# Optimization experiments

Hardware: AMD Instinct MI355X
Metric: run time of the kernel (lower is better)

Reference implementation:

```python
import jax, jax.numpy as jnp
import numpy as np

B, S, D, H, E = 8, 2048, 1024, 4096, 8


def setup_inputs() -> dict:
    key = jax.random.key(0)
    k0, k1, k2, k3 = jax.random.split(key, 4)
    x = jax.random.normal(k0, (B, S, D), dtype=jnp.float32)
    # hash-router assignment: one expert per token, shape [B, S, 1] (top-k dim k=1)
    assign = jax.random.randint(k1, (B, S, 1), 0, E, dtype=jnp.int64)
    # per-expert Linear(dim, hidden): W_e [E, D, H], b_e [E, H]
    W_e = jax.random.normal(k2, (E, D, H), dtype=jnp.float32) * (1.0 / np.sqrt(D))
    b_e = jnp.zeros((E, H), dtype=jnp.float32)
    # shared output Linear(hidden, dim)
    W_out = jax.random.normal(k3, (H, D), dtype=jnp.float32) * (1.0 / np.sqrt(H))
    b_out = jnp.zeros((D,), dtype=jnp.float32)
    return {"x": x, "W_e": W_e, "b_e": b_e, "W_out": W_out, "b_out": b_out,
            "assign": assign}


def reference(x, W_e, b_e, W_out, b_out, assign):
    num_experts = W_e.shape[0]
    hidden = W_e.shape[2]
    # zero-init combine buffer, matching torch.zeros(batch, seq, hidden)
    expert_out = jnp.zeros(x.shape[:2] + (hidden,), dtype=x.dtype)
    for e in range(num_experts):  # fixed small expert loop
        y = jnp.einsum("bsd,dh->bsh", x, W_e[e]) + b_e[e]
        mask = (assign == e).any(-1)  # [B, S]
        expert_out = jnp.where(mask[..., None], y, expert_out)
    h = jax.nn.relu(expert_out)
    return jnp.einsum("bsh,hd->bsd", h, W_out) + b_out
```

## Files before the change

### kernel.cpp

```cpp
#include <hip/hip_runtime.h>
#include <hip/hip_bf16.h>
#include <stdint.h>

#define NB 8
#define NS 2048
#define ND 1024
#define NH 4096
#define NE 8
#define NTOK (NB*NS)

typedef __bf16 bf16;
typedef bf16 bf16x8 __attribute__((ext_vector_type(8)));
typedef float f32x4 __attribute__((ext_vector_type(4)));

static const size_t OFF_XB  = 128 * 1024;
static const size_t OFF_WTE = OFF_XB  + (size_t)NTOK * ND * 2;
static const size_t OFF_WTO = OFF_WTE + (size_t)NE * NH * ND * 2;
static const size_t OFF_HB  = OFF_WTO + (size_t)ND * NH * 2;
static const size_t WS_NEED = OFF_HB  + (size_t)NTOK * NH * 2;

#define GLDS16(src, dst) __builtin_amdgcn_global_load_lds( \
    (__attribute__((address_space(1))) void*)(void*)(src), \
    (__attribute__((address_space(3))) void*)(dst), 16, 0, 0)


__global__ void k_route(const int* __restrict__ assign, int* __restrict__ meta) {
    __shared__ int cnt[NE];
    __shared__ int offs_s[NE];
    int tid = threadIdx.x;
    if (tid < NE) cnt[tid] = 0;
    __syncthreads();
    for (int t = tid; t < NTOK; t += 1024) atomicAdd(&cnt[assign[t] & 7], 1);
    __syncthreads();
    if (tid == 0) {
        int o = 0;
        for (int e = 0; e < NE; e++) {
            meta[e] = cnt[e]; meta[16 + e] = o; offs_s[e] = o; o += cnt[e];
        }
    }
    __syncthreads();
    if (tid < NE) cnt[tid] = offs_s[tid];
    __syncthreads();
    int* perm = meta + 512;
    for (int t = tid; t < NTOK; t += 1024) {
        int e = assign[t] & 7;
        int p = atomicAdd(&cnt[e], 1);
        perm[p] = t;
    }
}

__global__ void k_gather_cvt(const float* __restrict__ x, const int* __restrict__ meta,
                             bf16* __restrict__ xbp) {
    long i = (long)blockIdx.x * blockDim.x + threadIdx.x;
    int row = (int)(i >> 7);
    int c8  = (int)(i & 127);
    const int* perm = meta + 512;
    int tok = perm[row];
    const float4* s = (const float4*)(x + (size_t)tok * ND + c8 * 8);
    float4 v0 = s[0], v1 = s[1];
    bf16x8 o;
    o[0] = (bf16)v0.x; o[1] = (bf16)v0.y; o[2] = (bf16)v0.z; o[3] = (bf16)v0.w;
    o[4] = (bf16)v1.x; o[5] = (bf16)v1.y; o[6] = (bf16)v1.z; o[7] = (bf16)v1.w;
    *(bf16x8*)(xbp + i * 8) = o;
}

__global__ void k_transpose(const float* __restrict__ in, bf16* __restrict__ out,
                            int R, int C) {
    __shared__ float tile[32][33];
    int b  = blockIdx.z;
    int c0 = blockIdx.x * 32, r0 = blockIdx.y * 32;
    const float* inb = in + (size_t)b * R * C;
    bf16* outb = out + (size_t)b * R * C;
    int tx = threadIdx.x, ty = threadIdx.y;
#pragma unroll
    for (int i = 0; i < 4; i++) {
        int r = r0 + ty + i * 8;
        tile[ty + i * 8][tx] = inb[(size_t)r * C + c0 + tx];
    }
    __syncthreads();
#pragma unroll
    for (int i = 0; i < 4; i++) {
        int c = c0 + ty + i * 8;
        outb[(size_t)c * R + r0 + tx] = (bf16)tile[tx][ty + i * 8];
    }
}


#define BAR { __builtin_amdgcn_s_barrier(); asm volatile("" ::: "memory"); }
#define VMC8 asm volatile("s_waitcnt vmcnt(8)" ::: "memory")
#define VMC0 asm volatile("s_waitcnt vmcnt(0)" ::: "memory")

#define LDA(msub) { \
  const char* Ab = sm + abuf + wr * 16384; \
  _Pragma("unroll") for (int m = 0; m < 4; m++) { \
    int row = ((msub) * 4 + m) * 16 + lr; \
    af[m][0] = *(const bf16x8*)(Ab + row * 128 + xk0); \
    af[m][1] = *(const bf16x8*)(Ab + row * 128 + xk1); \
  } }

#define LDB(nsub) { \
  const char* Bb = sm + bbuf + (wc >> 1) * 16384; \
  _Pragma("unroll") for (int n = 0; n < 2; n++) { \
    int row = (wc & 1) * 64 + ((nsub) * 2 + n) * 16 + lr; \
    bfr[(nsub)*2+n][0] = *(const bf16x8*)(Bb + row * 128 + xk0); \
    bfr[(nsub)*2+n][1] = *(const bf16x8*)(Bb + row * 128 + xk1); \
  } }

#define MFMA_Q(msub, nsub) { \
  __builtin_amdgcn_s_setprio(1); \
  _Pragma("unroll") for (int m = 0; m < 4; m++) \
  _Pragma("unroll") for (int n = 0; n < 2; n++) \
  _Pragma("unroll") for (int k = 0; k < 2; k++) \
    acc[(msub)*4+m][(nsub)*2+n] = __builtin_amdgcn_mfma_f32_16x16x32_bf16( \
        af[m][k], bfr[(nsub)*2+n][k], acc[(msub)*4+m][(nsub)*2+n], 0, 0, 0); \
  __builtin_amdgcn_s_setprio(0); }

#define DO_TILE(i, S0, S1, S2, S3, VW) { \
  const int abuf = ((i) % 3) * 32768; \
  const int bbuf = 98304 + ((i) & 1) * 32768; \
  LDA(0); LDB(0); S0; BAR; MFMA_Q(0,0); BAR; \
  LDB(1);         S1; BAR; MFMA_Q(0,1); BAR; \
  LDA(1);         S2; BAR; MFMA_Q(1,0); BAR; \
                  S3; VW; BAR; MFMA_Q(1,1); BAR; \
}

#define STAGE_A(t, h) { \
    char* d = sm + ((t) % 3) * 32768 + (h) * 16384 + wid * 1024; \
    GLDS16(srcA(t, h, 0), d); \
    GLDS16(srcA(t, h, 1), d + 8192); }
#define STAGE_B(t, h) { \
    char* d = sm + 98304 + ((t) & 1) * 32768 + (h) * 16384 + wid * 1024; \
    GLDS16(srcB(t, h, 0), d); \
    GLDS16(srcB(t, h, 1), d + 8192); }

__launch_bounds__(512, 2)
__global__ void k_gemm1(const bf16* __restrict__ xbp, const bf16* __restrict__ wte,
                        const float* __restrict__ b_e, bf16* __restrict__ hb,
                        const int* __restrict__ meta) {
    __shared__ __align__(16) char sm[163840];
    int f = blockIdx.x;
    int e = f & 7, q = f >> 3;
    int j = q % 9, bx = q / 9;
    int cnt = meta[e];
    int rs  = meta[16 + e] + j * 256;
    int rc  = cnt - j * 256; if (rc > 256) rc = 256;
    if (rc <= 0) return;
    int n0 = bx * 256;

    int tid = threadIdx.x;
    int lane = tid & 63, wid = tid >> 6;
    int wr = wid >> 2, wc = wid & 3;
    int lr = lane & 15, kg = lane >> 4;
    int xk0 = (kg ^ (lr & 7)) * 16;
    int xk1 = ((4 + kg) ^ (lr & 7)) * 16;

    int sr = tid >> 3, sl = tid & 7;
    int g = sl ^ (sr & 7);
    const bf16* pa[2][2];
#pragma unroll
    for (int h = 0; h < 2; h++)
#pragma unroll
      for (int rr = 0; rr < 2; rr++) {
        int arow = h * 128 + rr * 64 + sr;
        int p = rs + (arow < rc - 1 ? arow : rc - 1);
        pa[h][rr] = xbp + (size_t)p * ND + g * 8;
      }
    const bf16* pb0 = wte + ((size_t)e * NH + n0 + sr) * ND + g * 8;

#define srcA(t, h, rr) (pa[h][rr] + (size_t)(t) * 64)
#define srcB(t, h, rr) (pb0 + ((h) * 128 + (rr) * 64) * (size_t)ND + (size_t)(t) * 64)

    f32x4 acc[8][4] = {};
    bf16x8 af[4][2], bfr[4][2];
    const int NT = ND / 64;

    STAGE_A(0, 0); STAGE_A(0, 1); STAGE_B(0, 0); STAGE_B(0, 1);
    STAGE_A(1, 0); STAGE_A(1, 1); STAGE_B(1, 0); STAGE_B(1, 1);
    VMC8;
    BAR;

#pragma unroll 6
    for (int i = 0; i < NT - 2; i++)
        DO_TILE(i, STAGE_A(i + 2, 0), STAGE_A(i + 2, 1),
                   STAGE_B(i + 2, 0), STAGE_B(i + 2, 1), VMC8);
    DO_TILE(NT - 2, , , , , VMC0);
    DO_TILE(NT - 1, , , , , );

    float bias[4];
#pragma unroll
    for (int n = 0; n < 4; n++) bias[n] = b_e[e * NH + n0 + wc * 64 + n * 16 + lr];
#pragma unroll
    for (int m = 0; m < 8; m++) {
#pragma unroll
        for (int rr = 0; rr < 4; rr++) {
            int row = wr * 128 + m * 16 + kg * 4 + rr;
            if (row < rc) {
                bf16* hp = hb + (size_t)(rs + row) * NH + n0 + wc * 64;
#pragma unroll
                for (int n = 0; n < 4; n++)
                    hp[n * 16 + lr] = (bf16)fmaxf(acc[m][n][rr] + bias[n], 0.0f);
            }
        }
    }
#undef srcA
#undef srcB
}

__launch_bounds__(512, 2)
__global__ void k_gemm2(const bf16* __restrict__ hb, const bf16* __restrict__ wto,
                        const float* __restrict__ b_out, const int* __restrict__ meta,
                        float* __restrict__ out) {
    __shared__ __align__(16) char sm[163840];
    int lin = blockIdx.x;
    int swz = (lin & 7) * 32 + (lin >> 3);
    int bx = swz & 3, by = swz >> 2;
    int m0 = by * 256, n0 = bx * 256;
    const int* perm = meta + 512;

    int tid = threadIdx.x;
    int lane = tid & 63, wid = tid >> 6;
    int wr = wid >> 2, wc = wid & 3;
    int lr = lane & 15, kg = lane >> 4;
    int xk0 = (kg ^ (lr & 7)) * 16;
    int xk1 = ((4 + kg) ^ (lr & 7)) * 16;

    int sr = tid >> 3, sl = tid & 7;
    int g = sl ^ (sr & 7);
    const bf16* pa0 = hb  + ((size_t)m0 + sr) * NH + g * 8;
    const bf16* pb0 = wto + ((size_t)n0 + sr) * NH + g * 8;

#define srcA(t, h, rr) (pa0 + ((h) * 128 + (rr) * 64) * (size_t)NH + (size_t)(t) * 64)
#define srcB(t, h, rr) (pb0 + ((h) * 128 + (rr) * 64) * (size_t)NH + (size_t)(t) * 64)

    f32x4 acc[8][4] = {};
    bf16x8 af[4][2], bfr[4][2];
    const int NT = NH / 64;

    STAGE_A(0, 0); STAGE_A(0, 1); STAGE_B(0, 0); STAGE_B(0, 1);
    STAGE_A(1, 0); STAGE_A(1, 1); STAGE_B(1, 0); STAGE_B(1, 1);
    VMC8;
    BAR;

#pragma unroll 6
    for (int i = 0; i < NT - 2; i++)
        DO_TILE(i, STAGE_A(i + 2, 0), STAGE_A(i + 2, 1),
                   STAGE_B(i + 2, 0), STAGE_B(i + 2, 1), VMC8);
    DO_TILE(NT - 2, , , , , VMC0);
    DO_TILE(NT - 1, , , , , );

    float bias[4];
#pragma unroll
    for (int n = 0; n < 4; n++) bias[n] = b_out[n0 + wc * 64 + n * 16 + lr];
#pragma unroll
    for (int m = 0; m < 8; m++) {
#pragma unroll
        for (int rr = 0; rr < 4; rr++) {
            int prow = m0 + wr * 128 + m * 16 + kg * 4 + rr;
            int tok = perm[prow];
            float* op = out + (size_t)tok * ND + n0 + wc * 64;
#pragma unroll
            for (int n = 0; n < 4; n++)
                op[n * 16 + lr] = acc[m][n][rr] + bias[n];
        }
    }
#undef srcA
#undef srcB
}

extern "C" void kernel_launch(void* const* d_in, const int* in_sizes, int n_in,
                              void* d_out, int out_size, void* d_ws, size_t ws_size,
                              hipStream_t stream) {
    const float* x     = (const float*)d_in[0];
    const float* W_e   = (const float*)d_in[1];
    const float* b_e   = (const float*)d_in[2];
    const float* W_out = (const float*)d_in[3];
    const float* b_out = (const float*)d_in[4];
    const int*   assign = (const int*)d_in[5];
    float* out = (float*)d_out;

    if (ws_size < WS_NEED) return;

    char* ws = (char*)d_ws;
    int*  meta = (int*)ws;
    bf16* xbp = (bf16*)(ws + OFF_XB);
    bf16* wte = (bf16*)(ws + OFF_WTE);
    bf16* wto = (bf16*)(ws + OFF_WTO);
    bf16* hb  = (bf16*)(ws + OFF_HB);

    k_route<<<1, 1024, 0, stream>>>(assign, meta);
    k_gather_cvt<<<NTOK * ND / (256 * 8), 256, 0, stream>>>(x, meta, xbp);
    k_transpose<<<dim3(NH / 32, ND / 32, NE), dim3(32, 8), 0, stream>>>(W_e, wte, ND, NH);
    k_transpose<<<dim3(ND / 32, NH / 32, 1), dim3(32, 8), 0, stream>>>(W_out, wto, NH, ND);
    k_gemm1<<<1152, 512, 0, stream>>>(xbp, wte, b_e, hb, meta);
    k_gemm2<<<256, 512, 0, stream>>>(hb, wto, b_out, meta, out);
}
```

Measured before the change: 438.0 us.

## Merge routing, x conversion and weight transposes into one prep kernel

Replaces four preprocessing launches with a single kernel whose blocks handle routing, contiguous x-to-bf16 conversion, or weight transpose tiles. The routing no longer serializes ahead of the gather, because gemm1 now reads x rows indirectly through the permutation instead of from a pre-permuted buffer. This removes launch gaps and the dependency between routing and conversion, but it makes gemm1's A loads scattered rows. The routing block is now a single 256-thread block among many. The gemm1 main loop unroll is also reduced from 6 to 2.

```diff
diff --git a/kernel.cpp b/kernel.cpp
--- a/kernel.cpp
+++ b/kernel.cpp
@@ -23,65 +23,68 @@
     (__attribute__((address_space(1))) void*)(void*)(src), \
     (__attribute__((address_space(3))) void*)(dst), 16, 0, 0)
 
-
-__global__ void k_route(const int* __restrict__ assign, int* __restrict__ meta) {
-    __shared__ int cnt[NE];
-    __shared__ int offs_s[NE];
+__global__ void k_prep(const int* __restrict__ assign, const float* __restrict__ x,
+                       const float* __restrict__ W_e, const float* __restrict__ W_out,
+                       int* __restrict__ meta, bf16* __restrict__ xb,
+                       bf16* __restrict__ wte, bf16* __restrict__ wto) {
+    int b = blockIdx.x;
     int tid = threadIdx.x;
-    if (tid < NE) cnt[tid] = 0;
-    __syncthreads();
-    for (int t = tid; t < NTOK; t += 1024) atomicAdd(&cnt[assign[t] & 7], 1);
-    __syncthreads();
-    if (tid == 0) {
-        int o = 0;
-        for (int e = 0; e < NE; e++) {
-            meta[e] = cnt[e]; meta[16 + e] = o; offs_s[e] = o; o += cnt[e];
-        }
-    }
-    __syncthreads();
-    if (tid < NE) cnt[tid] = offs_s[tid];
-    __syncthreads();
-    int* perm = meta + 512;
-    for (int t = tid; t < NTOK; t += 1024) {
-        int e = assign[t] & 7;
-        int p = atomicAdd(&cnt[e], 1);
-        perm[p] = t;
-    }
-}
-
-__global__ void k_gather_cvt(const float* __restrict__ x, const int* __restrict__ meta,
-                             bf16* __restrict__ xbp) {
-    long i = (long)blockIdx.x * blockDim.x + threadIdx.x;
-    int row = (int)(i >> 7);
-    int c8  = (int)(i & 127);
-    const int* perm = meta + 512;
-    int tok = perm[row];
-    const float4* s = (const float4*)(x + (size_t)tok * ND + c8 * 8);
-    float4 v0 = s[0], v1 = s[1];
-    bf16x8 o;
-    o[0] = (bf16)v0.x; o[1] = (bf16)v0.y; o[2] = (bf16)v0.z; o[3] = (bf16)v0.w;
-    o[4] = (bf16)v1.x; o[5] = (bf16)v1.y; o[6] = (bf16)v1.z; o[7] = (bf16)v1.w;
-    *(bf16x8*)(xbp + i * 8) = o;
-}
-
-__global__ void k_transpose(const float* __restrict__ in, bf16* __restrict__ out,
-                            int R, int C) {
+    if (b == 0) {
+        __shared__ int cnt[NE], cur[NE];
+        if (tid < NE) cnt[tid] = 0;
+        __syncthreads();
+        for (int t = tid; t < NTOK; t += 256) atomicAdd(&cnt[assign[t] & 7], 1);
+        __syncthreads();
+        if (tid == 0) {
+            int o = 0;
+            for (int e = 0; e < NE; e++) {
+                meta[e] = cnt[e]; meta[16 + e] = o; cur[e] = o; o += cnt[e];
+            }
+        }
+        __syncthreads();
+        int* perm = meta + 512;
+        for (int t = tid; t < NTOK; t += 256) {
+            int e = assign[t] & 7;
+            int p = atomicAdd(&cur[e], 1);
+            perm[p] = t;
+        }
+        return;
+    }
+    if (b <= 8192) {
+        long i = (long)(b - 1) * 256 + tid;
+        const float4* s = (const float4*)(x + i * 8);
+        float4 v0 = s[0], v1 = s[1];
+        bf16x8 o;
+        o[0] = (bf16)v0.x; o[1] = (bf16)v0.y; o[2] = (bf16)v0.z; o[3] = (bf16)v0.w;
+        o[4] = (bf16)v1.x; o[5] = (bf16)v1.y; o[6] = (bf16)v1.z; o[7] = (bf16)v1.w;
+        *(bf16x8*)(xb + i * 8) = o;
+        return;
+    }
     __shared__ float tile[32][33];
-    int b  = blockIdx.z;
-    int c0 = blockIdx.x * 32, r0 = blockIdx.y * 32;
-    const float* inb = in + (size_t)b * R * C;
-    bf16* outb = out + (size_t)b * R * C;
-    int tx = threadIdx.x, ty = threadIdx.y;
+    int idx = b - 8193;
+    const float* in; bf16* outp; int R, C, c0, r0;
+    if (idx < 32768) {
+        int z = idx >> 12, q = idx & 4095;
+        int bx = q & 127, by = q >> 7;
+        in = W_e + (size_t)z * ND * NH; outp = wte + (size_t)z * NH * ND;
+        R = ND; C = NH; c0 = bx * 32; r0 = by * 32;
+    } else {
+        int q = idx - 32768;
+        int bx = q & 31, by = q >> 5;
+        in = W_out; outp = wto;
+        R = NH; C = ND; c0 = bx * 32; r0 = by * 32;
+    }
+    int tx = tid & 31, ty = tid >> 5;
 #pragma unroll
     for (int i = 0; i < 4; i++) {
         int r = r0 + ty + i * 8;
-        tile[ty + i * 8][tx] = inb[(size_t)r * C + c0 + tx];
+        tile[ty + i * 8][tx] = in[(size_t)r * C + c0 + tx];
     }
     __syncthreads();
 #pragma unroll
     for (int i = 0; i < 4; i++) {
         int c = c0 + ty + i * 8;
-        outb[(size_t)c * R + r0 + tx] = (bf16)tile[tx][ty + i * 8];
+        outp[(size_t)c * R + r0 + tx] = (bf16)tile[tx][ty + i * 8];
     }
 }
 
@@ -134,18 +137,19 @@
     GLDS16(srcB(t, h, 1), d + 8192); }
 
 __launch_bounds__(512, 2)
-__global__ void k_gemm1(const bf16* __restrict__ xbp, const bf16* __restrict__ wte,
+__global__ void k_gemm1(const bf16* __restrict__ xb, const bf16* __restrict__ wte,
                         const float* __restrict__ b_e, bf16* __restrict__ hb,
                         const int* __restrict__ meta) {
     __shared__ __align__(16) char sm[163840];
     int f = blockIdx.x;
     int e = f & 7, q = f >> 3;
-    int j = q % 9, bx = q / 9;
+    int jj = q % 9, bx = q / 9;
     int cnt = meta[e];
-    int rs  = meta[16 + e] + j * 256;
-    int rc  = cnt - j * 256; if (rc > 256) rc = 256;
+    int rs  = meta[16 + e] + jj * 256;
+    int rc  = cnt - jj * 256; if (rc > 256) rc = 256;
     if (rc <= 0) return;
     int n0 = bx * 256;
+    const int* perm = meta + 512;
 
     int tid = threadIdx.x;
     int lane = tid & 63, wid = tid >> 6;
@@ -163,7 +167,7 @@
       for (int rr = 0; rr < 2; rr++) {
         int arow = h * 128 + rr * 64 + sr;
         int p = rs + (arow < rc - 1 ? arow : rc - 1);
-        pa[h][rr] = xbp + (size_t)p * ND + g * 8;
+        pa[h][rr] = xb + (size_t)perm[p] * ND + g * 8;
       }
     const bf16* pb0 = wte + ((size_t)e * NH + n0 + sr) * ND + g * 8;
 
@@ -179,7 +183,7 @@
     VMC8;
     BAR;
 
-#pragma unroll 6
+#pragma unroll 2
     for (int i = 0; i < NT - 2; i++)
         DO_TILE(i, STAGE_A(i + 2, 0), STAGE_A(i + 2, 1),
                    STAGE_B(i + 2, 0), STAGE_B(i + 2, 1), VMC8);
@@ -282,15 +286,12 @@
 
     char* ws = (char*)d_ws;
     int*  meta = (int*)ws;
-    bf16* xbp = (bf16*)(ws + OFF_XB);
+    bf16* xb  = (bf16*)(ws + OFF_XB);
     bf16* wte = (bf16*)(ws + OFF_WTE);
     bf16* wto = (bf16*)(ws + OFF_WTO);
     bf16* hb  = (bf16*)(ws + OFF_HB);
 
-    k_route<<<1, 1024, 0, stream>>>(assign, meta);
-    k_gather_cvt<<<NTOK * ND / (256 * 8), 256, 0, stream>>>(x, meta, xbp);
-    k_transpose<<<dim3(NH / 32, ND / 32, NE), dim3(32, 8), 0, stream>>>(W_e, wte, ND, NH);
-    k_transpose<<<dim3(ND / 32, NH / 32, 1), dim3(32, 8), 0, stream>>>(W_out, wto, NH, ND);
-    k_gemm1<<<1152, 512, 0, stream>>>(xbp, wte, b_e, hb, meta);
+    k_prep<<<45057, 256, 0, stream>>>(assign, x, W_e, W_out, meta, xb, wte, wto);
+    k_gemm1<<<1152, 512, 0, stream>>>(xb, wte, b_e, hb, meta);
     k_gemm2<<<256, 512, 0, stream>>>(hb, wto, b_out, meta, out);
 }
```

Result: faster. 412.7 us (-5.8%).
